# Kernel tuning notes

Hardware: AMD Instinct MI355X
Metric: run time of the kernel (lower is better)

Reference implementation:

```python
import jax, jax.numpy as jnp
import numpy as np

K = 32        # max neighbors per query point
RADIUS = 0.1  # ball radius
N1 = 8192
N2 = 8192


def setup_inputs() -> dict:
    key = jax.random.key(0)
    k1, k2 = jax.random.split(key)
    points1 = jax.random.uniform(k1, (1, N1, 3), dtype=jnp.float32)
    points2 = jax.random.uniform(k2, (1, N2, 3), dtype=jnp.float32)
    lengths1 = jnp.full((1,), N1, dtype=jnp.int32)  # unused by the kernel, kept for API parity
    lengths2 = jnp.full((1,), N2, dtype=jnp.int32)
    return {"points1": points1, "points2": points2, "lengths1": lengths1, "lengths2": lengths2}


def _ball_query(p1, p2, k, radius):
    # p1: [N1,3], p2: [N2,3]
    # squared distances via gram trick, no [N1,N2,3] diff tensor
    d2 = (jnp.sum(p1 * p1, axis=-1)[:, None]
          + jnp.sum(p2 * p2, axis=-1)[None, :]
          - 2.0 * (p1 @ p2.T))                                   # [N1,N2]
    within = d2 <= radius * radius                                # kernel skips only if dist > radius
    n2 = p2.shape[0]
    # pick the first k in-range neighbors in index order (deterministic stand-in
    # for the unspecified hash-grid traversal order)
    score = jnp.where(within, jnp.arange(n2, dtype=jnp.int32), n2)  # [N1,N2]
    _, idx = jax.lax.top_k(-score, k)                             # k smallest scores -> first k indices
    valid = jnp.take_along_axis(within, idx, axis=1)              # [N1,k]
    counts = jnp.minimum(jnp.sum(within, axis=-1), k).astype(jnp.int32)  # [N1]
    mapping = jnp.where(valid, idx, 0).astype(jnp.int32)          # zeros-padded like the torch buffer
    outputs = jnp.where(valid[..., None], p2[mapping], 0.0)       # [N1,k,3]
    return mapping, counts, outputs


def reference(points1, points2, lengths1, lengths2):
    mapping, num_neighbors, outputs = _ball_query(points1[0], points2[0], K, RADIUS)
    return mapping[None], num_neighbors[None], outputs[None]
```

## Files before the change

kernel.cpp:

```cpp
#include <hip/hip_runtime.h>

#define N1 8192
#define N2 8192
#define KNN 32
#define R2_F32 0.009999999776482582f

#define GDIM 10
#define NCELLS (GDIM * GDIM * GDIM)
#define CELL_W 0.109375f
#define INV_W  9.142857142857142f
#define CAP 40
#define HCAP 128
#define PRUNE2 0.0105f

#define WS_CNT 0
#define WS_PTS 4096

struct F3 { float x, y, z; };

__device__ __forceinline__ F3 ld3(const float* __restrict__ p, int j) {
    F3 r;
    r.x = p[3 * j + 0];
    r.y = p[3 * j + 1];
    r.z = p[3 * j + 2];
    return r;
}

__device__ __forceinline__ int cell_coord(float v) {
    int c = (int)(v * INV_W);
    return c > (GDIM - 1) ? (GDIM - 1) : c;
}

__device__ __forceinline__ int prefix_lt(unsigned long long m) {
    return (int)__builtin_amdgcn_mbcnt_hi(
        (unsigned)(m >> 32),
        __builtin_amdgcn_mbcnt_lo((unsigned)m, 0u));
}

__global__ __launch_bounds__(256) void k_build(const float* __restrict__ p2,
                                               int* __restrict__ cnt,
                                               float4* __restrict__ pts) {
    __shared__ float4 buf[4][CAP];
    __shared__ int    cl[4];
    const int w    = (int)(threadIdx.x >> 6);
    const int lane = (int)(threadIdx.x & 63);
    const int c    = (int)blockIdx.x;
    const int ccx = c / 100, ccy = (c / 10) % 10, ccz = c % 10;

    int count = 0;
    const int jofs = w * (N2 / 4);

    auto proc = [&](const F3& p, int jb) {
        const bool match = (cell_coord(p.x) == ccx) &&
                           (cell_coord(p.y) == ccy) &&
                           (cell_coord(p.z) == ccz);
        const unsigned long long m = __ballot(match);
        if (m) {
            const int pos = count + prefix_lt(m);
            if (match && pos < CAP)
                buf[w][pos] = make_float4(p.x, p.y, p.z, (float)(jb + lane));
            count += (int)__popcll(m);
        }
    };

    constexpr int NMB = (N2 / 4) / 256;
    F3 b0 = ld3(p2, jofs + 0 * 64 + lane);
    F3 b1 = ld3(p2, jofs + 1 * 64 + lane);
    F3 b2 = ld3(p2, jofs + 2 * 64 + lane);
    F3 b3 = ld3(p2, jofs + 3 * 64 + lane);
    for (int mb = 0; mb < NMB; ++mb) {
        const int nb = (mb + 1 < NMB) ? (mb + 1) : 0;
        F3 n0 = ld3(p2, jofs + nb * 256 + 0 * 64 + lane);
        F3 n1 = ld3(p2, jofs + nb * 256 + 1 * 64 + lane);
        F3 n2 = ld3(p2, jofs + nb * 256 + 2 * 64 + lane);
        F3 n3 = ld3(p2, jofs + nb * 256 + 3 * 64 + lane);
        const int jb = jofs + mb * 256;
        proc(b0, jb + 0 * 64);
        proc(b1, jb + 1 * 64);
        proc(b2, jb + 2 * 64);
        proc(b3, jb + 3 * 64);
        b0 = n0; b1 = n1; b2 = n2; b3 = n3;
    }

    if (lane == 0) cl[w] = count;
    __syncthreads();

    const int c0 = cl[0], c1 = cl[1], c2 = cl[2], c3 = cl[3];
    int start = 0;
    if (w > 0) start += c0;
    if (w > 1) start += c1;
    if (w > 2) start += c2;
    const int st = start < CAP ? start : CAP;
    int ns = CAP - st;
    if (count < ns) ns = count;
    if (lane < ns) pts[c * CAP + st + lane] = buf[w][lane];
    if (w == 0 && lane == 0) cnt[c] = c0 + c1 + c2 + c3;
}

__global__ __launch_bounds__(256) void k_query(
    const float* __restrict__ p1, const float4* __restrict__ pts,
    const int* __restrict__ cnt,
    float* __restrict__ map_f, float* __restrict__ cnt_f, float* __restrict__ out_f)
{
    __shared__ float4 hits[4][HCAP];
    __shared__ int cum_l[4][32];
    __shared__ int adj_l[4][32];
    const int w    = (int)(threadIdx.x >> 6);
    const int lane = (int)(threadIdx.x & 63);
    const int q    = (int)blockIdx.x * 4 + w;

    const float qx = p1[3 * q], qy = p1[3 * q + 1], qz = p1[3 * q + 2];
    const float s1 = __fadd_rn(__fadd_rn(__fmul_rn(qx, qx), __fmul_rn(qy, qy)),
                               __fmul_rn(qz, qz));

    const int cx = cell_coord(qx), cy = cell_coord(qy), cz = cell_coord(qz);

    int len = 0, id = 0;
    if (lane < 27) {
        const int ax = cx + lane / 9 - 1;
        const int ay = cy + (lane / 3) % 3 - 1;
        const int az = cz + lane % 3 - 1;
        const bool valid = (unsigned)ax < GDIM && (unsigned)ay < GDIM && (unsigned)az < GDIM;
        if (valid) {
            id = (ax * GDIM + ay) * GDIM + az;
            const float gx = fmaxf(0.0f, fmaxf((float)ax * CELL_W - qx, qx - (float)(ax + 1) * CELL_W));
            const float gy = fmaxf(0.0f, fmaxf((float)ay * CELL_W - qy, qy - (float)(ay + 1) * CELL_W));
            const float gz = fmaxf(0.0f, fmaxf((float)az * CELL_W - qz, qz - (float)(az + 1) * CELL_W));
            const float mind2 = gx * gx + gy * gy + gz * gz;
            if (mind2 <= PRUNE2) {
                int c = cnt[id];
                len = c < CAP ? c : CAP;
            }
        }
    }

    int cum = len;
#pragma unroll
    for (int d = 1; d < 32; d <<= 1) {
        const int v = __shfl_up(cum, d, 64);
        if (lane >= d) cum += v;
    }
    const int T = __shfl(cum, 26, 64);
    if (lane < 32) {
        cum_l[w][lane] = cum;
        adj_l[w][lane] = id * CAP - (cum - len);
    }

    int hcnt = 0;
    for (int g0 = 0; g0 < T; g0 += 64) {
        const int g = g0 + lane;
        const bool active = g < T;
        int lo = 0;
#pragma unroll
        for (int st = 16; st > 0; st >>= 1)
            if (cum_l[w][lo + st - 1] <= g) lo += st;
        float4 e = make_float4(2.0f, 2.0f, 2.0f, 0.0f);
        if (active) e = pts[g + adj_l[w][lo]];
        const float s2  = __fadd_rn(__fadd_rn(__fmul_rn(e.x, e.x), __fmul_rn(e.y, e.y)),
                                    __fmul_rn(e.z, e.z));
        const float dot = __fmaf_rn(qz, e.z, __fmaf_rn(qy, e.y, __fmul_rn(qx, e.x)));
        const float d2  = __fsub_rn(__fadd_rn(s1, s2), __fadd_rn(dot, dot));
        const bool within = active && (d2 <= R2_F32);
        const unsigned long long m = __ballot(within);
        if (m) {
            const int pos = hcnt + prefix_lt(m);
            if (within && pos < HCAP) hits[w][pos] = e;
            hcnt += (int)__popcll(m);
        }
    }

    const int cap2 = hcnt < HCAP ? hcnt : HCAP;
    int k0 = 0x7FFFFFFF, k1 = 0x7FFFFFFF;
    if (lane < cap2)      k0 = (((int)hits[w][lane].w) << 7) | lane;
    if (lane + 64 < cap2) k1 = (((int)hits[w][lane + 64].w) << 7) | (lane + 64);
    for (int k = 2; k <= 128; k <<= 1) {
        for (int s = k >> 1; s > 0; s >>= 1) {
            if (s == 64) {
                const int lo2 = k0 < k1 ? k0 : k1;
                const int hi2 = k0 < k1 ? k1 : k0;
                k0 = lo2; k1 = hi2;
            } else {
                const int p0 = __shfl_xor(k0, s, 64);
                const int p1 = __shfl_xor(k1, s, 64);
                const bool lower = (lane & s) == 0;
                const bool asc0  = ((lane     ) & k) == 0;
                const bool asc1  = ((lane + 64) & k) == 0;
                k0 = (lower == asc0) ? (k0 < p0 ? k0 : p0) : (k0 > p0 ? k0 : p0);
                k1 = (lower == asc1) ? (k1 < p1 ? k1 : p1) : (k1 > p1 ? k1 : p1);
            }
        }
    }

    const int outc = hcnt < KNN ? hcnt : KNN;
    if (lane < KNN) {
        const int s = q * KNN + lane;
        float* o = out_f + s * 3;
        if (lane < outc) {
            const float4 e = hits[w][k0 & 127];
            map_f[s] = (float)(k0 >> 7);
            o[0] = e.x; o[1] = e.y; o[2] = e.z;
        } else {
            map_f[s] = 0.0f;
            o[0] = 0.0f; o[1] = 0.0f; o[2] = 0.0f;
        }
    }
    if (lane == 0) cnt_f[q] = (float)outc;
}

extern "C" void kernel_launch(void* const* d_in, const int* in_sizes, int n_in,
                              void* d_out, int out_size, void* d_ws, size_t ws_size,
                              hipStream_t stream) {
    const float* p1 = (const float*)d_in[0];
    const float* p2 = (const float*)d_in[1];
    float* out = (float*)d_out;

    float* map_f = out;
    float* cnt_f = out + (size_t)N1 * KNN;
    float* out_f = cnt_f + N1;

    char* ws = (char*)d_ws;
    int*    cnt = (int*)(ws + WS_CNT);
    float4* pts = (float4*)(ws + WS_PTS);

    hipLaunchKernelGGL(k_build, dim3(NCELLS), dim3(256), 0, stream, p2, cnt, pts);
    hipLaunchKernelGGL(k_query, dim3(N1 / 4), dim3(256), 0, stream,
                       p1, pts, cnt, map_f, cnt_f, out_f);
}
```

Measured before the change: 21.79 us.

## Replace bitonic sort with rank counting and use shuffles for cell lookup

The 128-element bitonic sort of hit indices is replaced by a rank computation: each lane counts how many hits have a smaller point index by scanning the hit list in LDS, then scatters its hit directly to that output slot. The per-cell prefix and offset tables move from LDS arrays into registers and are read with wave shuffles in the binary search. This removes the many shuffle-and-compare sort stages and some LDS traffic, at the cost of a serial loop over the hit count with LDS broadcast reads, plus scattered global writes instead of ordered ones.

After: 21.23 us. -2.5%, faster.

```diff
diff --git a/kernel.cpp b/kernel.cpp
--- a/kernel.cpp
+++ b/kernel.cpp
@@ -103,8 +103,6 @@
     float* __restrict__ map_f, float* __restrict__ cnt_f, float* __restrict__ out_f)
 {
     __shared__ float4 hits[4][HCAP];
-    __shared__ int cum_l[4][32];
-    __shared__ int adj_l[4][32];
     const int w    = (int)(threadIdx.x >> 6);
     const int lane = (int)(threadIdx.x & 63);
     const int q    = (int)blockIdx.x * 4 + w;
@@ -141,10 +139,7 @@
         if (lane >= d) cum += v;
     }
     const int T = __shfl(cum, 26, 64);
-    if (lane < 32) {
-        cum_l[w][lane] = cum;
-        adj_l[w][lane] = id * CAP - (cum - len);
-    }
+    const int adj = id * CAP - (cum - len);
 
     int hcnt = 0;
     for (int g0 = 0; g0 < T; g0 += 64) {
@@ -152,10 +147,13 @@
         const bool active = g < T;
         int lo = 0;
 #pragma unroll
-        for (int st = 16; st > 0; st >>= 1)
-            if (cum_l[w][lo + st - 1] <= g) lo += st;
+        for (int st = 16; st > 0; st >>= 1) {
+            const int v = __shfl(cum, lo + st - 1, 64);
+            if (v <= g) lo += st;
+        }
+        const int aj = __shfl(adj, lo, 64);
         float4 e = make_float4(2.0f, 2.0f, 2.0f, 0.0f);
-        if (active) e = pts[g + adj_l[w][lo]];
+        if (active) e = pts[g + aj];
         const float s2  = __fadd_rn(__fadd_rn(__fmul_rn(e.x, e.x), __fmul_rn(e.y, e.y)),
                                     __fmul_rn(e.z, e.z));
         const float dot = __fmaf_rn(qz, e.z, __fmaf_rn(qy, e.y, __fmul_rn(qx, e.x)));
@@ -170,39 +168,36 @@
     }
 
     const int cap2 = hcnt < HCAP ? hcnt : HCAP;
-    int k0 = 0x7FFFFFFF, k1 = 0x7FFFFFFF;
-    if (lane < cap2)      k0 = (((int)hits[w][lane].w) << 7) | lane;
-    if (lane + 64 < cap2) k1 = (((int)hits[w][lane + 64].w) << 7) | (lane + 64);
-    for (int k = 2; k <= 128; k <<= 1) {
-        for (int s = k >> 1; s > 0; s >>= 1) {
-            if (s == 64) {
-                const int lo2 = k0 < k1 ? k0 : k1;
-                const int hi2 = k0 < k1 ? k1 : k0;
-                k0 = lo2; k1 = hi2;
-            } else {
-                const int p0 = __shfl_xor(k0, s, 64);
-                const int p1 = __shfl_xor(k1, s, 64);
-                const bool lower = (lane & s) == 0;
-                const bool asc0  = ((lane     ) & k) == 0;
-                const bool asc1  = ((lane + 64) & k) == 0;
-                k0 = (lower == asc0) ? (k0 < p0 ? k0 : p0) : (k0 > p0 ? k0 : p0);
-                k1 = (lower == asc1) ? (k1 < p1 ? k1 : p1) : (k1 > p1 ? k1 : p1);
-            }
-        }
+    float4 e0, e1;
+    int j0 = 0x7FFFFFFF, j1 = 0x7FFFFFFF;
+    if (lane < cap2)      { e0 = hits[w][lane];      j0 = (int)e0.w; }
+    if (lane + 64 < cap2) { e1 = hits[w][lane + 64]; j1 = (int)e1.w; }
+    int r0 = 0, r1 = 0;
+#pragma unroll 4
+    for (int i = 0; i < cap2; ++i) {
+        const int ji = (int)hits[w][i].w;
+        r0 += (ji < j0) ? 1 : 0;
+        r1 += (ji < j1) ? 1 : 0;
     }
 
     const int outc = hcnt < KNN ? hcnt : KNN;
-    if (lane < KNN) {
+    if (lane < cap2 && r0 < KNN) {
+        const int s = q * KNN + r0;
+        map_f[s] = e0.w;
+        float* o = out_f + s * 3;
+        o[0] = e0.x; o[1] = e0.y; o[2] = e0.z;
+    }
+    if (lane + 64 < cap2 && r1 < KNN) {
+        const int s = q * KNN + r1;
+        map_f[s] = e1.w;
+        float* o = out_f + s * 3;
+        o[0] = e1.x; o[1] = e1.y; o[2] = e1.z;
+    }
+    if (lane < KNN && lane >= outc) {
         const int s = q * KNN + lane;
+        map_f[s] = 0.0f;
         float* o = out_f + s * 3;
-        if (lane < outc) {
-            const float4 e = hits[w][k0 & 127];
-            map_f[s] = (float)(k0 >> 7);
-            o[0] = e.x; o[1] = e.y; o[2] = e.z;
-        } else {
-            map_f[s] = 0.0f;
-            o[0] = 0.0f; o[1] = 0.0f; o[2] = 0.0f;
-        }
+        o[0] = 0.0f; o[1] = 0.0f; o[2] = 0.0f;
     }
     if (lane == 0) cnt_f[q] = (float)outc;
 }
```
